# Kernel tuning notes

Hardware: AMD Instinct MI355X
Metric: run time of the kernel (lower is better)

## Reference

```python
import jax, jax.numpy as jnp
import numpy as np

CL1_K = 25
CL2_K = 25


def cheb_stack(L, x0, K):
    # x0: (V, M) -> (K, V, M) Chebyshev basis T_k(L) x0
    if K == 1:
        return x0[None]
    x1 = L @ x0
    if K == 2:
        return jnp.stack([x0, x1])

    def step(carry, _):
        xm1, xm2 = carry
        xk = 2.0 * (L @ xm1) - xm2
        return (xk, xm1), xk

    _, rest = jax.lax.scan(step, (x1, x0), None, length=K - 2)
    return jnp.concatenate([x0[None], x1[None], rest], axis=0)


def graph_conv(x, L, W, b, K):
    # x: (B, C, V) -> (B, Fout, V); matches torch Graph_Conv permute/view logic
    B, C, V = x.shape
    x0 = x.transpose(2, 1, 0).reshape(V, C * B)
    xs = cheb_stack(L, x0, K)                              # (K, V, C*B)
    xs = xs.reshape(K, V, C, B).transpose(3, 1, 2, 0)      # (B, V, C, K)
    xs = xs.reshape(B * V, C * K)
    y = xs @ W.T + b                                       # (B*V, Fout)
    return y.reshape(B, V, -1).transpose(0, 2, 1)


def maxpool4(x):
    B, C, V = x.shape
    return x.reshape(B, C, V // 4, 4).max(axis=-1)


def setup_inputs() -> dict:
    key = jax.random.key(0)
    ks = jax.random.split(key, 10)
    B, C, V, Vp = 32, 16, 4000, 4096
    CL1_F, CL2_F, FC_F = 64, 128, 10
    x = jax.random.normal(ks[0], (B, C, V), dtype=jnp.float32)
    perm = jax.random.permutation(ks[1], Vp)
    # rescaled Laplacians, scaled for stable 25-step recurrence
    L1 = jax.random.normal(ks[2], (Vp, Vp), dtype=jnp.float32) * (0.3 / np.sqrt(Vp))
    L2 = jax.random.normal(ks[3], (Vp // 4, Vp // 4), dtype=jnp.float32) * (0.3 / np.sqrt(Vp // 4))
    W1 = jax.random.normal(ks[4], (CL1_F, C * CL1_K), dtype=jnp.float32) * np.sqrt(2.0 / (C * CL1_K + CL1_F))
    b1 = jnp.zeros((CL1_F,), dtype=jnp.float32)
    W2 = jax.random.normal(ks[5], (CL2_F, CL1_F * CL2_K), dtype=jnp.float32) * np.sqrt(2.0 / (CL1_F * CL2_K + CL2_F))
    b2 = jnp.zeros((CL2_F,), dtype=jnp.float32)
    FC_IN = CL2_F * Vp // 16
    Wfc = jax.random.normal(ks[6], (FC_F, FC_IN), dtype=jnp.float32) * np.sqrt(2.0 / (FC_IN + FC_F))
    bfc = jnp.zeros((FC_F,), dtype=jnp.float32)
    return {"x": x, "perm": perm, "L1": L1, "L2": L2, "W1": W1, "b1": b1,
            "W2": W2, "b2": b2, "Wfc": Wfc, "bfc": bfc}


def reference(x, perm, L1, L2, W1, b1, W2, b2, Wfc, bfc):
    # BatchNorm1d(affine=False), training-mode batch statistics
    mu = x.mean(axis=(0, 2), keepdims=True)
    var = x.var(axis=(0, 2), keepdims=True)
    x = (x - mu) / jnp.sqrt(var + 1e-5)
    # Permute: zero-pad vertices to len(perm), then index
    B, C, V = x.shape
    Vp = perm.shape[0]
    x = jnp.pad(x, ((0, 0), (0, 0), (0, Vp - V)))[:, :, perm]
    x = jax.nn.relu(graph_conv(x, L1, W1, b1, CL1_K))
    x = maxpool4(x)
    x = jax.nn.relu(graph_conv(x, L2, W2, b2, CL2_K))
    x = maxpool4(x)
    x = x.reshape(B, -1)
    # dropout in eval mode (identity)
    return x @ Wfc.T + bfc
```

## Files before the change

### kernel.cpp

```cpp
#include <hip/hip_runtime.h>

typedef _Float16 half8 __attribute__((ext_vector_type(8)));
typedef _Float16 half4 __attribute__((ext_vector_type(4)));
typedef float f32x4 __attribute__((ext_vector_type(4)));

__device__ __forceinline__ void gload_lds16(const void* g, void* l) {
  __builtin_amdgcn_global_load_lds((const __attribute__((address_space(1))) void*)g,
                                   (__attribute__((address_space(3))) void*)l, 16, 0, 0);
}

__global__ __launch_bounds__(256) void k_bn_partial(const float* __restrict__ x,
                                                    float* __restrict__ part) {
  const int c = blockIdx.x & 15;
  const int seg = blockIdx.x >> 4;
  const int t = threadIdx.x;
  float s = 0.f, s2 = 0.f;
  for (int b = 0; b < 32; ++b) {
    const float* row = x + (size_t)(b * 16 + c) * 4000 + seg * 500;
    for (int v = t; v < 500; v += 256) {
      float val = row[v];
      s += val;
      s2 += val * val;
    }
  }
#pragma unroll
  for (int off = 32; off > 0; off >>= 1) {
    s += __shfl_down(s, off);
    s2 += __shfl_down(s2, off);
  }
  __shared__ float rs_[4], rs2_[4];
  if ((t & 63) == 0) { rs_[t >> 6] = s; rs2_[t >> 6] = s2; }
  __syncthreads();
  if (t == 0) {
    part[c * 8 + seg] = rs_[0] + rs_[1] + rs_[2] + rs_[3];
    part[128 + c * 8 + seg] = rs2_[0] + rs2_[1] + rs2_[2] + rs2_[3];
  }
}

__global__ void k_bn_final(const float* __restrict__ part, float* __restrict__ musig) {
  const int c = threadIdx.x;
  if (c < 16) {
    float S = 0.f, S2 = 0.f;
#pragma unroll
    for (int seg = 0; seg < 8; ++seg) {
      S += part[c * 8 + seg];
      S2 += part[128 + c * 8 + seg];
    }
    const float inv = 1.f / 128000.f;
    float mu = S * inv;
    float var = S2 * inv - mu * mu;
    musig[c] = mu;
    musig[16 + c] = rsqrtf(var + 1e-5f);
  }
}

__global__ __launch_bounds__(256) void k_build_x0(const float* __restrict__ x,
                                                  const int* __restrict__ perm,
                                                  const float* __restrict__ musig,
                                                  _Float16* __restrict__ X0) {
  const int idx = blockIdx.x * 256 + threadIdx.x;
  const int v = idx & 4095;
  const int m = idx >> 12;
  const int b = m & 31;
  const int c = m >> 5;
  const int pv = perm[v];
  float val = 0.f;
  if (pv < 4000)
    val = (x[((size_t)(b * 16 + c)) * 4000 + pv] - musig[c]) * musig[16 + c] * 0.0625f;
  X0[idx] = (_Float16)val;
}

__global__ __launch_bounds__(256) void k_cvt_f16(const float* __restrict__ s,
                                                 _Float16* __restrict__ d, int n) {
  const int i = (blockIdx.x * 256 + threadIdx.x) * 4;
  if (i >= n) return;
  f32x4 v = *(const f32x4*)(s + i);
  half4 h;
  h[0] = (_Float16)v[0]; h[1] = (_Float16)v[1];
  h[2] = (_Float16)v[2]; h[3] = (_Float16)v[3];
  *(half4*)(d + i) = h;
}

__global__ __launch_bounds__(256) void k_prep_w(const float* __restrict__ W,
                                                _Float16* __restrict__ Wp,
                                                int F, int shiftC) {
  const int idx = blockIdx.x * 256 + threadIdx.x;
  const int CS = 1 << shiftC;
  const int KPtot = 26 * CS;
  if (idx >= F * KPtot) return;
  const int f = idx / KPtot;
  const int rem = idx - f * KPtot;
  const int k = rem >> shiftC;
  const int c = rem & (CS - 1);
  float v = 0.f;
  if (k < 25) v = W[(size_t)f * (CS * 25) + c * 25 + k];
  Wp[idx] = (_Float16)v;
}

__global__ __launch_bounds__(512, 2) void k_cheb(const _Float16* __restrict__ Xprev,
                                                 const _Float16* __restrict__ Lm,
                                                 const _Float16* __restrict__ Xm2,
                                                 _Float16* __restrict__ Xout,
                                                 int V, float alpha, float beta) {
  __shared__ _Float16 lds[2][2][12288];
  const int t = threadIdx.x;
  const int lane = t & 63;
  const int w = t >> 6;
  const int kh = w >> 2;
  const int wl = w & 3;
  const int wr = wl >> 1, wc = wl & 1;
  const int v0 = blockIdx.x * 64;
  const int m0 = blockIdx.y * 128;
  const size_t rs = (size_t)V * 2;
  const int K2 = V >> 1;
  const int NT2 = K2 >> 6;

  const char* Ag = (const char*)Xprev + (size_t)m0 * rs + (size_t)kh * K2 * 2;
  const char* Bg = (const char*)Lm + (size_t)v0 * rs + (size_t)kh * K2 * 2;
  const size_t soff = (size_t)(lane >> 3) * rs + (size_t)(((lane & 7) * 16) ^ ((lane >> 3) << 4));

  f32x4 acc[4][2] = {};

  auto stage = [&](int buf, int tt) {
    const char* ag = Ag + (size_t)tt * 128 + soff;
    const char* bg = Bg + (size_t)tt * 128 + soff;
    char* A = (char*)&lds[kh][buf][0];
    char* B = (char*)&lds[kh][buf][8192];
#pragma unroll
    for (int j = 0; j < 4; ++j) {
      const int r0 = wl * 32 + j * 8;
      gload_lds16(ag + (size_t)r0 * rs, A + r0 * 128);
    }
#pragma unroll
    for (int j = 0; j < 2; ++j) {
      const int r0 = wl * 16 + j * 8;
      gload_lds16(bg + (size_t)r0 * rs, B + r0 * 128);
    }
  };

  stage(0, 0);

  for (int tt = 0; tt < NT2; ++tt) {
    const int cur = tt & 1;
    if (tt + 1 < NT2) {
      stage(cur ^ 1, tt + 1);
      asm volatile("s_waitcnt vmcnt(6)" ::: "memory");
    } else {
      asm volatile("s_waitcnt vmcnt(0)" ::: "memory");
    }
    asm volatile("s_barrier" ::: "memory");
    const char* A = (const char*)&lds[kh][cur][0];
    const char* B = (const char*)&lds[kh][cur][8192];
#pragma unroll
    for (int kk = 0; kk < 2; ++kk) {
      const int cb = kk * 64 + ((lane >> 4) << 4);
      half8 a[4], b[2];
#pragma unroll
      for (int mi = 0; mi < 4; ++mi) {
        const int ar = wr * 64 + mi * 16 + (lane & 15);
        a[mi] = *(const half8*)(A + ar * 128 + (cb ^ ((ar & 7) << 4)));
      }
#pragma unroll
      for (int ni = 0; ni < 2; ++ni) {
        const int br = wc * 32 + ni * 16 + (lane & 15);
        b[ni] = *(const half8*)(B + br * 128 + (cb ^ ((br & 7) << 4)));
      }
#pragma unroll
      for (int mi = 0; mi < 4; ++mi)
#pragma unroll
        for (int ni = 0; ni < 2; ++ni)
          acc[mi][ni] = __builtin_amdgcn_mfma_f32_16x16x32_f16(a[mi], b[ni], acc[mi][ni], 0, 0, 0);
    }
    asm volatile("s_barrier" ::: "memory");
  }

  __syncthreads();
  float* red = (float*)&lds[0][0][0];
  if (kh == 1) {
    float* dst = red + wl * 2048 + lane * 4;
#pragma unroll
    for (int mi = 0; mi < 4; ++mi)
#pragma unroll
      for (int ni = 0; ni < 2; ++ni)
        *(f32x4*)(dst + (mi * 2 + ni) * 256) = acc[mi][ni];
  }
  __syncthreads();
  if (kh == 0) {
    const float* src = red + wl * 2048 + lane * 4;
    const int rbase = (lane >> 4) << 2;
#pragma unroll
    for (int mi = 0; mi < 4; ++mi) {
#pragma unroll
      for (int ni = 0; ni < 2; ++ni) {
        f32x4 o = *(const f32x4*)(src + (mi * 2 + ni) * 256);
        const int vv = v0 + wc * 32 + ni * 16 + (lane & 15);
#pragma unroll
        for (int r = 0; r < 4; ++r) {
          const int mm = m0 + wr * 64 + mi * 16 + rbase + r;
          const size_t idx = (size_t)mm * V + vv;
          float val = alpha * (acc[mi][ni][r] + o[r]);
          if (beta != 0.f) val -= (float)Xm2[idx];
          Xout[idx] = (_Float16)val;
        }
      }
    }
  }
}

__global__ __launch_bounds__(256, 2) void k_dense(const _Float16* __restrict__ Wp,
                                                  const _Float16* __restrict__ XS,
                                                  const float* __restrict__ bias,
                                                  float* __restrict__ Yt,
                                                  int Vv, int shiftC, int nsteps,
                                                  size_t planeV, int Ntot,
                                                  float ascale, float bscale) {
  __shared__ _Float16 Alds[64 * 32];
  __shared__ _Float16 Blds[32 * 64];
  const int t = threadIdx.x;
  const int lane = t & 63;
  const int w = t >> 6;
  const int n0 = blockIdx.x * 64;
  const int f0 = blockIdx.y * 64;
  const int b = n0 / Vv;
  const int vb = n0 % Vv;
  const int KP = nsteps * 32;
  const int cmask = (1 << shiftC) - 1;

  f32x4 acc0 = {0.f, 0.f, 0.f, 0.f}, acc1 = {0.f, 0.f, 0.f, 0.f};
  f32x4 acc2 = {0.f, 0.f, 0.f, 0.f}, acc3 = {0.f, 0.f, 0.f, 0.f};

  for (int s = 0; s < nsteps; ++s) {
    const int q0 = s * 32;
    {
      const int row = t >> 2, cb = (t & 3) * 16;
      half8 v = *(const half8*)((const char*)Wp + ((size_t)(f0 + row) * KP + q0) * 2 + cb);
      *(half8*)((char*)Alds + row * 64 + cb) = v;
    }
    {
      const int q = q0 + (t >> 3), cb = (t & 7) * 16;
      const int k = q >> shiftC, c = q & cmask;
      half8 v = {};
      if (k < 25)
        v = *(const half8*)((const char*)XS +
                            ((size_t)k * planeV + (size_t)(c * 32 + b) * Vv + vb) * 2 + cb);
      *(half8*)((char*)Blds + (t >> 3) * 128 + cb) = v;
    }
    __syncthreads();
    half8 a0 = *(const half8*)((char*)Alds + ((lane & 15) + 0) * 64 + ((lane >> 4) << 4));
    half8 a1 = *(const half8*)((char*)Alds + ((lane & 15) + 16) * 64 + ((lane >> 4) << 4));
    half8 a2 = *(const half8*)((char*)Alds + ((lane & 15) + 32) * 64 + ((lane >> 4) << 4));
    half8 a3 = *(const half8*)((char*)Alds + ((lane & 15) + 48) * 64 + ((lane >> 4) << 4));
    half8 bf;
    const int col = (w << 4) + (lane & 15);
#pragma unroll
    for (int j = 0; j < 8; ++j)
      bf[j] = Blds[(((lane >> 4) << 3) + j) * 64 + col];
    acc0 = __builtin_amdgcn_mfma_f32_16x16x32_f16(a0, bf, acc0, 0, 0, 0);
    acc1 = __builtin_amdgcn_mfma_f32_16x16x32_f16(a1, bf, acc1, 0, 0, 0);
    acc2 = __builtin_amdgcn_mfma_f32_16x16x32_f16(a2, bf, acc2, 0, 0, 0);
    acc3 = __builtin_amdgcn_mfma_f32_16x16x32_f16(a3, bf, acc3, 0, 0, 0);
    __syncthreads();
  }

  const int n = n0 + (w << 4) + (lane & 15);
  f32x4 accs[4] = {acc0, acc1, acc2, acc3};
#pragma unroll
  for (int mi = 0; mi < 4; ++mi) {
#pragma unroll
    for (int r = 0; r < 4; ++r) {
      const int f = f0 + (mi << 4) + ((lane >> 4) << 2) + r;
      float val = ascale * accs[mi][r] + bscale * bias[f];
      Yt[(size_t)f * Ntot + n] = fmaxf(val, 0.f);
    }
  }
}

__global__ __launch_bounds__(256) void k_pool1(const float* __restrict__ Yt,
                                               _Float16* __restrict__ X2) {
  const int idx = blockIdx.x * 256 + threadIdx.x;
  const int v2 = idx & 1023;
  const int rest = idx >> 10;
  const int b = rest & 31;
  const int f = rest >> 5;
  f32x4 q = *(const f32x4*)(Yt + (size_t)f * 131072 + b * 4096 + v2 * 4);
  float mx = fmaxf(fmaxf(q[0], q[1]), fmaxf(q[2], q[3]));
  X2[(size_t)(f * 32 + b) * 1024 + v2] = (_Float16)(mx * 0.015625f);
}

__global__ __launch_bounds__(256) void k_pool2(const float* __restrict__ Yt,
                                               float* __restrict__ p2) {
  const int idx = blockIdx.x * 256 + threadIdx.x;
  const int v3 = idx & 255;
  const int rest = idx >> 8;
  const int f = rest & 127;
  const int b = rest >> 7;
  f32x4 q = *(const f32x4*)(Yt + (size_t)f * 32768 + b * 1024 + v3 * 4);
  float mx = fmaxf(fmaxf(q[0], q[1]), fmaxf(q[2], q[3]));
  p2[(size_t)b * 32768 + f * 256 + v3] = mx;
}

__global__ __launch_bounds__(256) void k_fc_part(const float* __restrict__ p2,
                                                 const float* __restrict__ Wfc,
                                                 float* __restrict__ partF) {
  const int b = blockIdx.x >> 3;
  const int seg = blockIdx.x & 7;
  const int t = threadIdx.x;
  const int lane = t & 63;
  const int w = t >> 6;
  const int base = seg * 4096;
  float acc[10];
#pragma unroll
  for (int o = 0; o < 10; ++o) acc[o] = 0.f;
  const float* pb = p2 + (size_t)b * 32768 + base;
  for (int i = t; i < 4096; i += 256) {
    float p = pb[i];
#pragma unroll
    for (int o = 0; o < 10; ++o) acc[o] += p * Wfc[(size_t)o * 32768 + base + i];
  }
#pragma unroll
  for (int off = 32; off > 0; off >>= 1)
#pragma unroll
    for (int o = 0; o < 10; ++o) acc[o] += __shfl_down(acc[o], off);
  __shared__ float rws[10][4];
  if (lane == 0) {
#pragma unroll
    for (int o = 0; o < 10; ++o) rws[o][w] = acc[o];
  }
  __syncthreads();
  if (t < 10) partF[blockIdx.x * 10 + t] =
      rws[t][0] + rws[t][1] + rws[t][2] + rws[t][3];
}

__global__ void k_fc_final(const float* __restrict__ partF,
                           const float* __restrict__ bfc,
                           float* __restrict__ out) {
  const int t = threadIdx.x;
  if (t < 320) {
    const int b = t / 10, o = t - b * 10;
    float s = 0.f;
#pragma unroll
    for (int seg = 0; seg < 8; ++seg) s += partF[(b * 8 + seg) * 10 + o];
    out[b * 10 + o] = 64.f * s + bfc[o];
  }
}

extern "C" void kernel_launch(void* const* d_in, const int* in_sizes, int n_in,
                              void* d_out, int out_size, void* d_ws, size_t ws_size,
                              hipStream_t stream) {
  (void)in_sizes; (void)n_in; (void)out_size; (void)ws_size;
  const float* x = (const float*)d_in[0];
  const int* perm = (const int*)d_in[1];
  const float* L1 = (const float*)d_in[2];
  const float* L2 = (const float*)d_in[3];
  const float* W1 = (const float*)d_in[4];
  const float* b1 = (const float*)d_in[5];
  const float* W2 = (const float*)d_in[6];
  const float* b2 = (const float*)d_in[7];
  const float* Wfc = (const float*)d_in[8];
  const float* bfc = (const float*)d_in[9];
  float* out = (float*)d_out;

  char* ws = (char*)d_ws;
  size_t off = 0;
  auto alloc = [&](size_t bytes) {
    char* p = ws + off;
    off += (bytes + 255) & ~(size_t)255;
    return p;
  };
  _Float16* L1h = (_Float16*)alloc(16777216ull * 2);
  _Float16* L2h = (_Float16*)alloc(1048576ull * 2);
  _Float16* W1p = (_Float16*)alloc(64ull * 416 * 2);
  _Float16* W2p = (_Float16*)alloc(128ull * 1664 * 2);
  float* part = (float*)alloc(256 * 4);
  float* musig = (float*)alloc(32 * 4);
  float* partF = (float*)alloc(2560 * 4);
  _Float16* XS = (_Float16*)alloc(25ull * 2097152 * 2);
  float* Yt = (float*)alloc(64ull * 131072 * 4);
  float* p2 = (float*)alloc(32ull * 128 * 256 * 4);

  k_cvt_f16<<<16384, 256, 0, stream>>>(L1, L1h, 16777216);
  k_cvt_f16<<<1024, 256, 0, stream>>>(L2, L2h, 1048576);
  k_prep_w<<<104, 256, 0, stream>>>(W1, W1p, 64, 4);
  k_prep_w<<<832, 256, 0, stream>>>(W2, W2p, 128, 6);
  k_bn_partial<<<128, 256, 0, stream>>>(x, part);
  k_bn_final<<<1, 64, 0, stream>>>(part, musig);
  k_build_x0<<<8192, 256, 0, stream>>>(x, perm, musig, XS);

  const size_t plane = 2097152;
  for (int k = 1; k < 25; ++k) {
    k_cheb<<<dim3(64, 4), 512, 0, stream>>>(
        XS + (size_t)(k - 1) * plane, L1h,
        XS + (size_t)(k >= 2 ? k - 2 : 0) * plane, XS + (size_t)k * plane,
        4096, (k == 1) ? 1.f : 2.f, (k == 1) ? 0.f : 1.f);
  }
  k_dense<<<dim3(2048, 1), 256, 0, stream>>>(W1p, XS, b1, Yt, 4096, 4, 13, plane,
                                             131072, 16.f, 1.f);
  k_pool1<<<8192, 256, 0, stream>>>(Yt, XS);
  for (int k = 1; k < 25; ++k) {
    k_cheb<<<dim3(16, 16), 512, 0, stream>>>(
        XS + (size_t)(k - 1) * plane, L2h,
        XS + (size_t)(k >= 2 ? k - 2 : 0) * plane, XS + (size_t)k * plane,
        1024, (k == 1) ? 1.f : 2.f, (k == 1) ? 0.f : 1.f);
  }
  k_dense<<<dim3(512, 2), 256, 0, stream>>>(W2p, XS, b2, Yt, 1024, 6, 52, plane,
                                            32768, 1.f, 0.015625f);
  k_pool2<<<4096, 256, 0, stream>>>(Yt, p2);
  k_fc_part<<<256, 256, 0, stream>>>(p2, Wfc, partF);
  k_fc_final<<<1, 320, 0, stream>>>(partF, bfc, out);
}
```

Before: 1.293 ms.

## Split-K the layer-1 Chebyshev GEMM with a separate reduction kernel, pad dense LDS

Replaces the layer-1 Chebyshev step kernel with a 4-way split-K GEMM (256 blocks, 128x256 tiles, swizzled LDS, double-buffered async global-to-LDS loads) that writes fp16 partials, followed by a small reduction kernel that applies the recurrence. The aim is better occupancy of the CUs, since the old grid only had 256 blocks each doing the full K. The dense kernel also gets padded LDS strides to reduce bank conflicts, and the W1 packing is rounded to 28 k-steps to match. The trade-off is extra partial-buffer traffic, an added launch per step, and fp16 rounding of the partial sums.

After: 1.202 ms. 7.0% less time.

```diff
diff --git a/kernel.cpp b/kernel.cpp
--- a/kernel.cpp
+++ b/kernel.cpp
@@ -83,10 +83,10 @@
 
 __global__ __launch_bounds__(256) void k_prep_w(const float* __restrict__ W,
                                                 _Float16* __restrict__ Wp,
-                                                int F, int shiftC) {
+                                                int F, int shiftC, int kround) {
   const int idx = blockIdx.x * 256 + threadIdx.x;
   const int CS = 1 << shiftC;
-  const int KPtot = 26 * CS;
+  const int KPtot = kround * CS;
   if (idx >= F * KPtot) return;
   const int f = idx / KPtot;
   const int rem = idx - f * KPtot;
@@ -95,6 +95,117 @@
   float v = 0.f;
   if (k < 25) v = W[(size_t)f * (CS * 25) + c * 25 + k];
   Wp[idx] = (_Float16)v;
+}
+
+__global__ __launch_bounds__(512, 1) void k_cheb_ks(const _Float16* __restrict__ Xprev,
+                                                    const _Float16* __restrict__ Lm,
+                                                    _Float16* __restrict__ P) {
+  __shared__ _Float16 lds[2][24576];
+  const int t = threadIdx.x;
+  const int lane = t & 63;
+  const int w = t >> 6;
+  const int wm = w >> 2, wn = w & 3;
+  const int bid = blockIdx.x;
+  const int bx = bid & 15;
+  const int by = (bid >> 4) & 3;
+  const int kq = bid >> 6;
+  const int v0 = bx * 256, m0 = by * 128;
+  const size_t rs = 8192;
+
+  const char* Ag = (const char*)Xprev + (size_t)m0 * rs + (size_t)kq * 2048;
+  const char* Bg = (const char*)Lm + (size_t)v0 * rs + (size_t)kq * 2048;
+  const size_t soff = (size_t)(lane >> 3) * rs + (size_t)(((lane & 7) * 16) ^ ((lane >> 3) << 4));
+
+  f32x4 acc[4][4] = {};
+
+  auto stage = [&](int buf, int tt) {
+    const char* ag = Ag + (size_t)tt * 128 + soff;
+    const char* bg = Bg + (size_t)tt * 128 + soff;
+    char* A = (char*)&lds[buf][0];
+    char* B = (char*)&lds[buf][8192];
+#pragma unroll
+    for (int j = 0; j < 2; ++j) {
+      const int r0 = w * 16 + j * 8;
+      gload_lds16(ag + (size_t)r0 * rs, A + r0 * 128);
+    }
+#pragma unroll
+    for (int j = 0; j < 4; ++j) {
+      const int r0 = w * 32 + j * 8;
+      gload_lds16(bg + (size_t)r0 * rs, B + r0 * 128);
+    }
+  };
+
+  stage(0, 0);
+
+  const int NT = 16;
+  for (int tt = 0; tt < NT; ++tt) {
+    const int cur = tt & 1;
+    if (tt + 1 < NT) {
+      stage(cur ^ 1, tt + 1);
+      asm volatile("s_waitcnt vmcnt(6)" ::: "memory");
+    } else {
+      asm volatile("s_waitcnt vmcnt(0)" ::: "memory");
+    }
+    asm volatile("s_barrier" ::: "memory");
+    const char* A = (const char*)&lds[cur][0];
+    const char* B = (const char*)&lds[cur][8192];
+#pragma unroll
+    for (int kk = 0; kk < 2; ++kk) {
+      const int cb = kk * 64 + ((lane >> 4) << 4);
+      half8 a[4], b[4];
+#pragma unroll
+      for (int mi = 0; mi < 4; ++mi) {
+        const int ar = wm * 64 + mi * 16 + (lane & 15);
+        a[mi] = *(const half8*)(A + ar * 128 + (cb ^ ((ar & 7) << 4)));
+      }
+#pragma unroll
+      for (int ni = 0; ni < 4; ++ni) {
+        const int br = wn * 64 + ni * 16 + (lane & 15);
+        b[ni] = *(const half8*)(B + br * 128 + (cb ^ ((br & 7) << 4)));
+      }
+#pragma unroll
+      for (int mi = 0; mi < 4; ++mi)
+#pragma unroll
+        for (int ni = 0; ni < 4; ++ni)
+          acc[mi][ni] = __builtin_amdgcn_mfma_f32_16x16x32_f16(a[mi], b[ni], acc[mi][ni], 0, 0, 0);
+    }
+    asm volatile("s_barrier" ::: "memory");
+  }
+
+  _Float16* Pq = P + (size_t)kq * 2097152;
+  const int rbase = (lane >> 4) << 2;
+#pragma unroll
+  for (int mi = 0; mi < 4; ++mi) {
+#pragma unroll
+    for (int ni = 0; ni < 4; ++ni) {
+      const int vv = v0 + wn * 64 + ni * 16 + (lane & 15);
+#pragma unroll
+      for (int r = 0; r < 4; ++r) {
+        const int mm = m0 + wm * 64 + mi * 16 + rbase + r;
+        Pq[(size_t)mm * 4096 + vv] = (_Float16)acc[mi][ni][r];
+      }
+    }
+  }
+}
+
+__global__ __launch_bounds__(256) void k_cheb_red(const _Float16* __restrict__ P,
+                                                  const _Float16* __restrict__ Xm2,
+                                                  _Float16* __restrict__ Xout,
+                                                  float alpha, float beta) {
+  const int i = (blockIdx.x * 256 + threadIdx.x) * 8;
+  half8 p0 = *(const half8*)(P + i);
+  half8 p1 = *(const half8*)(P + 2097152 + i);
+  half8 p2 = *(const half8*)(P + 4194304 + i);
+  half8 p3 = *(const half8*)(P + 6291456 + i);
+  half8 xm2 = {};
+  if (beta != 0.f) xm2 = *(const half8*)(Xm2 + i);
+  half8 o;
+#pragma unroll
+  for (int j = 0; j < 8; ++j) {
+    float s = (float)p0[j] + (float)p1[j] + (float)p2[j] + (float)p3[j];
+    o[j] = (_Float16)(alpha * s - beta * (float)xm2[j]);
+  }
+  *(half8*)(Xout + i) = o;
 }
 
 __global__ __launch_bounds__(512, 2) void k_cheb(const _Float16* __restrict__ Xprev,
@@ -214,8 +325,8 @@
                                                   int Vv, int shiftC, int nsteps,
                                                   size_t planeV, int Ntot,
                                                   float ascale, float bscale) {
-  __shared__ _Float16 Alds[64 * 32];
-  __shared__ _Float16 Blds[32 * 64];
+  __shared__ _Float16 Alds[64 * 40];
+  __shared__ _Float16 Blds[32 * 66];
   const int t = threadIdx.x;
   const int lane = t & 63;
   const int w = t >> 6;
@@ -234,7 +345,7 @@
     {
       const int row = t >> 2, cb = (t & 3) * 16;
       half8 v = *(const half8*)((const char*)Wp + ((size_t)(f0 + row) * KP + q0) * 2 + cb);
-      *(half8*)((char*)Alds + row * 64 + cb) = v;
+      *(half8*)((char*)Alds + row * 80 + cb) = v;
     }
     {
       const int q = q0 + (t >> 3), cb = (t & 7) * 16;
@@ -243,18 +354,21 @@
       if (k < 25)
         v = *(const half8*)((const char*)XS +
                             ((size_t)k * planeV + (size_t)(c * 32 + b) * Vv + vb) * 2 + cb);
-      *(half8*)((char*)Blds + (t >> 3) * 128 + cb) = v;
+      uint4 uv = *(uint4*)&v;
+      uint* ud = (uint*)((char*)Blds + (t >> 3) * 132 + cb);
+      ud[0] = uv.x; ud[1] = uv.y; ud[2] = uv.z; ud[3] = uv.w;
     }
     __syncthreads();
-    half8 a0 = *(const half8*)((char*)Alds + ((lane & 15) + 0) * 64 + ((lane >> 4) << 4));
-    half8 a1 = *(const half8*)((char*)Alds + ((lane & 15) + 16) * 64 + ((lane >> 4) << 4));
-    half8 a2 = *(const half8*)((char*)Alds + ((lane & 15) + 32) * 64 + ((lane >> 4) << 4));
-    half8 a3 = *(const half8*)((char*)Alds + ((lane & 15) + 48) * 64 + ((lane >> 4) << 4));
+    const int g16 = (lane >> 4) << 4;
+    half8 a0 = *(const half8*)((char*)Alds + ((lane & 15) + 0) * 80 + g16);
+    half8 a1 = *(const half8*)((char*)Alds + ((lane & 15) + 16) * 80 + g16);
+    half8 a2 = *(const half8*)((char*)Alds + ((lane & 15) + 32) * 80 + g16);
+    half8 a3 = *(const half8*)((char*)Alds + ((lane & 15) + 48) * 80 + g16);
     half8 bf;
     const int col = (w << 4) + (lane & 15);
 #pragma unroll
     for (int j = 0; j < 8; ++j)
-      bf[j] = Blds[(((lane >> 4) << 3) + j) * 64 + col];
+      bf[j] = Blds[(((lane >> 4) << 3) + j) * 66 + col];
     acc0 = __builtin_amdgcn_mfma_f32_16x16x32_f16(a0, bf, acc0, 0, 0, 0);
     acc1 = __builtin_amdgcn_mfma_f32_16x16x32_f16(a1, bf, acc1, 0, 0, 0);
     acc2 = __builtin_amdgcn_mfma_f32_16x16x32_f16(a2, bf, acc2, 0, 0, 0);
@@ -369,31 +483,32 @@
   };
   _Float16* L1h = (_Float16*)alloc(16777216ull * 2);
   _Float16* L2h = (_Float16*)alloc(1048576ull * 2);
-  _Float16* W1p = (_Float16*)alloc(64ull * 416 * 2);
+  _Float16* W1p = (_Float16*)alloc(64ull * 448 * 2);
   _Float16* W2p = (_Float16*)alloc(128ull * 1664 * 2);
   float* part = (float*)alloc(256 * 4);
   float* musig = (float*)alloc(32 * 4);
   float* partF = (float*)alloc(2560 * 4);
   _Float16* XS = (_Float16*)alloc(25ull * 2097152 * 2);
+  _Float16* Pq = (_Float16*)alloc(4ull * 2097152 * 2);
   float* Yt = (float*)alloc(64ull * 131072 * 4);
   float* p2 = (float*)alloc(32ull * 128 * 256 * 4);
 
   k_cvt_f16<<<16384, 256, 0, stream>>>(L1, L1h, 16777216);
   k_cvt_f16<<<1024, 256, 0, stream>>>(L2, L2h, 1048576);
-  k_prep_w<<<104, 256, 0, stream>>>(W1, W1p, 64, 4);
-  k_prep_w<<<832, 256, 0, stream>>>(W2, W2p, 128, 6);
+  k_prep_w<<<112, 256, 0, stream>>>(W1, W1p, 64, 4, 28);
+  k_prep_w<<<832, 256, 0, stream>>>(W2, W2p, 128, 6, 26);
   k_bn_partial<<<128, 256, 0, stream>>>(x, part);
   k_bn_final<<<1, 64, 0, stream>>>(part, musig);
   k_build_x0<<<8192, 256, 0, stream>>>(x, perm, musig, XS);
 
   const size_t plane = 2097152;
   for (int k = 1; k < 25; ++k) {
-    k_cheb<<<dim3(64, 4), 512, 0, stream>>>(
-        XS + (size_t)(k - 1) * plane, L1h,
-        XS + (size_t)(k >= 2 ? k - 2 : 0) * plane, XS + (size_t)k * plane,
-        4096, (k == 1) ? 1.f : 2.f, (k == 1) ? 0.f : 1.f);
-  }
-  k_dense<<<dim3(2048, 1), 256, 0, stream>>>(W1p, XS, b1, Yt, 4096, 4, 13, plane,
+    k_cheb_ks<<<256, 512, 0, stream>>>(XS + (size_t)(k - 1) * plane, L1h, Pq);
+    k_cheb_red<<<1024, 256, 0, stream>>>(
+        Pq, XS + (size_t)(k >= 2 ? k - 2 : 0) * plane, XS + (size_t)k * plane,
+        (k == 1) ? 1.f : 2.f, (k == 1) ? 0.f : 1.f);
+  }
+  k_dense<<<dim3(2048, 1), 256, 0, stream>>>(W1p, XS, b1, Yt, 4096, 4, 14, plane,
                                              131072, 16.f, 1.f);
   k_pool1<<<8192, 256, 0, stream>>>(Yt, XS);
   for (int k = 1; k < 25; ++k) {
```
